# Optimization experiments

Measured on AMD Instinct MI355X. Metric: run time of the kernel, lower is better.

The kernel has to match this reference:

```python
import jax, jax.numpy as jnp
import numpy as np

B, H0, W0, C = 16, 56, 56, 96
NH, WS, SS = 3, 7, 3
HID, NCL, TAU = 384, 128, 0.5
EPS = 1e-6

def layernorm(x, g, b):
    m = jnp.mean(x, -1, keepdims=True)
    v = jnp.mean((x - m) ** 2, -1, keepdims=True)
    return (x - m) * jax.lax.rsqrt(v + 1e-5) * g + b

def setup_inputs() -> dict:
    key = jax.random.key(0)
    ks = jax.random.split(key, 16)
    s = lambda d: 1.0 / np.sqrt(d)
    return {
        "x": jax.random.normal(ks[0], (B, H0 * W0, C), jnp.float32),
        "norm1_g": jnp.ones((C,)), "norm1_b": jnp.zeros((C,)),
        "qkv_w": jax.random.normal(ks[1], (3 * C, C)) * s(C),
        "qkv_b": jnp.zeros((3 * C,)),
        "proj_w": jax.random.normal(ks[2], (C, C)) * s(C),
        "proj_b": jnp.zeros((C,)),
        "norm2_g": jnp.ones((C,)), "norm2_b": jnp.zeros((C,)),
        "ffn_norm_g": jnp.ones((C,)), "ffn_norm_b": jnp.zeros((C,)),
        "pin_w": jax.random.normal(ks[3], (HID, C)) * s(C),
        "pin_b": jnp.zeros((HID,)),
        "tm_inc": jax.random.normal(ks[4], (NCL, 2 * HID)) * 0.5,
        "tm_out": jax.random.normal(ks[5], (NCL, C)) * s(NCL),
        "gate": jnp.float32(0.5),
        "H": H0, "W": W0,
    }

def window_attention(win, qkv_w, qkv_b, proj_w, proj_b):
    N, T, Cc = win.shape
    hd = Cc // NH
    qkv = win @ qkv_w.T + qkv_b                      # [N, T, 3C]
    qkv = qkv.reshape(N, T, 3, NH, hd).transpose(2, 0, 3, 1, 4)
    q, k, v = qkv[0], qkv[1], qkv[2]                 # [N, nh, T, hd]
    attn = jax.nn.softmax(jnp.einsum('nhqd,nhkd->nhqk', q, k) * (hd ** -0.5), axis=-1)
    out = jnp.einsum('nhqk,nhkd->nhqd', attn, v).transpose(0, 2, 1, 3).reshape(N, T, Cc)
    return out @ proj_w.T + proj_b

def tm_ffn(x, ffn_norm_g, ffn_norm_b, pin_w, pin_b, tm_inc, tm_out, gate):
    # x: [B, T, C]
    Bb, T, Cc = x.shape
    y = jax.nn.sigmoid(layernorm(x, ffn_norm_g, ffn_norm_b) @ pin_w.T + pin_b)  # [B,T,HID]
    flat = y.reshape(Bb * T, HID)
    lits = jnp.clip(jnp.concatenate([flat, 1.0 - flat], axis=-1), EPS, 1.0)     # [N, 2*HID]
    m = jax.nn.sigmoid(tm_inc)
    hard = (m > TAU).astype(m.dtype)
    m_ste = m + jax.lax.stop_gradient(hard - m)      # binary via STE
    # binary mask -> conjunction prod_k l_k^{m_jk} = exp(log(l) @ m^T)
    clauses = jnp.exp(jnp.log(lits) @ m_ste.T)       # [N, NCL]
    logits = (clauses @ tm_out).reshape(Bb, T, Cc)
    g = jax.nn.sigmoid(gate)
    return g * logits + (1.0 - g) * jax.nn.sigmoid(logits)

def reference(x, norm1_g, norm1_b, qkv_w, qkv_b, proj_w, proj_b,
              norm2_g, norm2_b, ffn_norm_g, ffn_norm_b,
              pin_w, pin_b, tm_inc, tm_out, gate, H, W):
    Bb, L, Cc = x.shape
    shortcut = x
    y = layernorm(x, norm1_g, norm1_b).reshape(Bb, H, W, Cc)
    pad_h = (WS - H % WS) % WS
    pad_w = (WS - W % WS) % WS
    if pad_h or pad_w:
        y = jnp.pad(y, ((0, 0), (0, pad_h), (0, pad_w), (0, 0)))
    Hp, Wp = y.shape[1], y.shape[2]
    if SS > 0:
        y = jnp.roll(y, shift=(-SS, -SS), axis=(1, 2))
    # window partition
    y = y.reshape(Bb, Hp // WS, WS, Wp // WS, WS, Cc).transpose(0, 1, 3, 2, 4, 5)
    win = y.reshape(-1, WS * WS, Cc)
    a = window_attention(win, qkv_w, qkv_b, proj_w, proj_b)
    a = a.reshape(Bb, Hp // WS, Wp // WS, WS, WS, Cc)
    if SS > 0:
        a = jnp.roll(a, shift=(SS, SS), axis=(3, 4))
    # window reverse
    a = a.transpose(0, 1, 3, 2, 4, 5).reshape(Bb, Hp, Wp, Cc)
    if pad_h or pad_w:
        a = a[:, :H, :W, :]
    a = a.reshape(Bb, H * W, Cc)
    x1 = shortcut + a
    x2 = x1 + tm_ffn(layernorm(x1, norm2_g, norm2_b),
                     ffn_norm_g, ffn_norm_b, pin_w, pin_b, tm_inc, tm_out, gate)
    return x2
```

## Files before the change

### kernel.cpp

```cpp
#include <hip/hip_runtime.h>

#define NB 16
#define NHH 56
#define NWW 56
#define NC 96
#define NL (NHH*NWW)
#define NTOK (NB*NL)
#define WSZ 7
#define NT 49
#define SSH 3
#define NWIN 1024
#define HDIM 32
#define HID_ 384
#define NCL_ 128
#define NLIT 768
#define EPS_ 1e-6f
#define LOG_EPS -13.815510558f

typedef unsigned short u16;
typedef unsigned int   u32;
typedef __attribute__((ext_vector_type(8))) short short8;
typedef __attribute__((ext_vector_type(4))) float f32x4;

__device__ __forceinline__ float us2f(u16 u) {
  union { u32 u; float f; } x; x.u = ((u32)u) << 16; return x.f;
}
__device__ __forceinline__ u16 f2us(float f) {
  union { float f; u32 u; } x; x.f = f;
  u32 lsb = (x.u >> 16) & 1u;
  return (u16)((x.u + 0x7fffu + lsb) >> 16);
}
__device__ __forceinline__ float sigmoidf_(float x) { return 1.f / (1.f + __expf(-x)); }

__global__ __launch_bounds__(256) void k0_prep(const float* __restrict__ tm_inc,
                                               const float* __restrict__ pin_w,
                                               const float* __restrict__ tm_out,
                                               const float* __restrict__ qkv_w,
                                               const float* __restrict__ proj_w,
                                               u16* __restrict__ maskb,
                                               u16* __restrict__ pinwb,
                                               u16* __restrict__ tmoT,
                                               u16* __restrict__ qkvwb,
                                               u16* __restrict__ projwb) {
  int idx = blockIdx.x * 256 + threadIdx.x;
  if (idx < NCL_ * NLIT) {
    int c = idx / NLIT, q = idx - c * NLIT;
    int j = (q & 1) ? (q >> 1) + HID_ : (q >> 1);
    maskb[idx] = (tm_inc[(size_t)c * NLIT + j] > 0.f) ? (u16)0x3F80 : (u16)0;
  }
  if (idx < HID_ * NC)
    pinwb[idx] = f2us(pin_w[idx]);
  if (idx < NC * NCL_) {
    int c = idx / NCL_, k = idx - c * NCL_;
    tmoT[idx] = f2us(tm_out[(size_t)k * NC + c]);
  }
  if (idx < 3 * NC * NC)
    qkvwb[idx] = f2us(qkv_w[idx]);
  if (idx < NC * NC)
    projwb[idx] = f2us(proj_w[idx]);
}

__global__ __launch_bounds__(256, 4) void k2_attn(const float* __restrict__ x,
                                               const float* __restrict__ n1g,
                                               const float* __restrict__ n1b,
                                               const u16* __restrict__ qkvwb,
                                               const float* __restrict__ qkv_b,
                                               const u16* __restrict__ projwb,
                                               const float* __restrict__ proj_b,
                                               float* __restrict__ x1) {
  __shared__ __align__(16) u16 syb[64 * 104];
  __shared__ __align__(16) u16 sk [64 * 104];
  __shared__ __align__(16) u16 svT[96 * 72];
  const int tid  = threadIdx.x;
  const int wave = tid >> 6;
  const int lane = tid & 63;
  const int l16  = lane & 15;
  const int quad = lane >> 4;
  const int win  = blockIdx.x;
  const int t0   = wave * 16;
  const int bb = win >> 6, wl = win & 63;
  const int hbase = (wl >> 3) * WSZ, wbase = (wl & 7) * WSZ;

  {
    const int t = tid >> 2, s = tid & 3;
    if (t < NT) {
      int hp = hbase + t / WSZ, wp = wbase + t % WSZ;
      int h = hp + SSH; if (h >= NHH) h -= NHH;
      int w = wp + SSH; if (w >= NWW) w -= NWW;
      const float* xp = x + ((size_t)bb * NL + (size_t)h * NWW + w) * NC;
      float4 v[6];
      float sum = 0.f;
      #pragma unroll
      for (int k = 0; k < 6; ++k) {
        v[k] = *reinterpret_cast<const float4*>(xp + s * 4 + k * 16);
        sum += v[k].x + v[k].y + v[k].z + v[k].w;
      }
      sum += __shfl_xor(sum, 1); sum += __shfl_xor(sum, 2);
      float mean = sum * (1.f / 96.f);
      float ssq = 0.f;
      #pragma unroll
      for (int k = 0; k < 6; ++k) {
        float d0 = v[k].x - mean, d1 = v[k].y - mean;
        float d2 = v[k].z - mean, d3 = v[k].w - mean;
        ssq += d0 * d0 + d1 * d1 + d2 * d2 + d3 * d3;
      }
      ssq += __shfl_xor(ssq, 1); ssq += __shfl_xor(ssq, 2);
      float rstd = rsqrtf(ssq * (1.f / 96.f) + 1e-5f);
      #pragma unroll
      for (int k = 0; k < 6; ++k) {
        int c = s * 4 + k * 16;
        const float4 g4 = *reinterpret_cast<const float4*>(n1g + c);
        const float4 b4 = *reinterpret_cast<const float4*>(n1b + c);
        syb[t * 104 + c + 0] = f2us((v[k].x - mean) * rstd * g4.x + b4.x);
        syb[t * 104 + c + 1] = f2us((v[k].y - mean) * rstd * g4.y + b4.y);
        syb[t * 104 + c + 2] = f2us((v[k].z - mean) * rstd * g4.z + b4.z);
        syb[t * 104 + c + 3] = f2us((v[k].w - mean) * rstd * g4.w + b4.w);
      }
    } else {
      #pragma unroll
      for (int k = 0; k < 6; ++k) {
        int c = s * 4 + k * 16;
        syb[t * 104 + c + 0] = 0; syb[t * 104 + c + 1] = 0;
        syb[t * 104 + c + 2] = 0; syb[t * 104 + c + 3] = 0;
      }
    }
  }

  {
    short8 afr[3];
    #pragma unroll
    for (int ks = 0; ks < 3; ++ks)
      afr[ks] = *reinterpret_cast<const short8*>(&syb[(t0 + l16) * 104 + quad * 8 + ks * 32]);
    short8 rb[4][3];
    #pragma unroll
    for (int p = 0; p < 4; ++p)
      #pragma unroll
      for (int ks = 0; ks < 3; ++ks)
        rb[p][ks] = *reinterpret_cast<const short8*>(
            qkvwb + (size_t)(p * 16 + l16) * NC + quad * 8 + ks * 32);
    #pragma unroll
    for (int nt = 0; nt < 18; ++nt) {
      const int n0 = nt * 16;
      const float bias = qkv_b[n0 + l16];
      short8 b0 = rb[nt & 3][0], b1 = rb[nt & 3][1], b2 = rb[nt & 3][2];
      if (nt + 4 < 18) {
        #pragma unroll
        for (int ks = 0; ks < 3; ++ks)
          rb[nt & 3][ks] = *reinterpret_cast<const short8*>(
              qkvwb + (size_t)((nt + 4) * 16 + l16) * NC + quad * 8 + ks * 32);
      }
      f32x4 acc = {0.f, 0.f, 0.f, 0.f};
      acc = __builtin_amdgcn_mfma_f32_16x16x32_bf16(afr[0], b0, acc, 0, 0, 0);
      acc = __builtin_amdgcn_mfma_f32_16x16x32_bf16(afr[1], b1, acc, 0, 0, 0);
      acc = __builtin_amdgcn_mfma_f32_16x16x32_bf16(afr[2], b2, acc, 0, 0, 0);
      const int part = nt / 6;
      const int oc = n0 - part * 96 + l16;
      if (part < 2) {
        u16* dst = (part == 0) ? syb : sk;
        #pragma unroll
        for (int r = 0; r < 4; ++r)
          dst[(t0 + quad * 4 + r) * 104 + oc] = f2us(acc[r] + bias);
      } else {
        #pragma unroll
        for (int r = 0; r < 4; ++r)
          svT[oc * 72 + (t0 + quad * 4 + r)] = f2us(acc[r] + bias);
      }
    }
  }
  __syncthreads();

  u16* spw = sk + wave * 16 * 72;
  const float sscale = 0.17677669529663687f;
  short8 qf[3];
  f32x4 s[3][4];
  #pragma unroll
  for (int h = 0; h < 3; ++h)
    qf[h] = *reinterpret_cast<const short8*>(&syb[(t0 + l16) * 104 + h * HDIM + quad * 8]);
  #pragma unroll
  for (int h = 0; h < 3; ++h) {
    const int d0 = h * HDIM;
    #pragma unroll
    for (int nt = 0; nt < 4; ++nt) {
      short8 kf = *reinterpret_cast<const short8*>(&sk[(nt * 16 + l16) * 104 + d0 + quad * 8]);
      f32x4 a = {0.f, 0.f, 0.f, 0.f};
      s[h][nt] = __builtin_amdgcn_mfma_f32_16x16x32_bf16(qf[h], kf, a, 0, 0, 0);
    }
  }
  __syncthreads();
  #pragma unroll
  for (int h = 0; h < 3; ++h) {
    const int d0 = h * HDIM;
    #pragma unroll
    for (int nt = 0; nt < 4; ++nt)
      #pragma unroll
      for (int r = 0; r < 4; ++r) s[h][nt][r] *= sscale;
    if (l16 >= 1) {
      #pragma unroll
      for (int r = 0; r < 4; ++r) s[h][3][r] = -1e30f;
    }
    #pragma unroll
    for (int r = 0; r < 4; ++r) {
      float m = fmaxf(fmaxf(s[h][0][r], s[h][1][r]), fmaxf(s[h][2][r], s[h][3][r]));
      #pragma unroll
      for (int off = 8; off > 0; off >>= 1) m = fmaxf(m, __shfl_xor(m, off, 16));
      float e0 = __expf(s[h][0][r] - m), e1 = __expf(s[h][1][r] - m);
      float e2 = __expf(s[h][2][r] - m), e3 = __expf(s[h][3][r] - m);
      float sum = e0 + e1 + e2 + e3;
      #pragma unroll
      for (int off = 8; off > 0; off >>= 1) sum += __shfl_xor(sum, off, 16);
      float inv = 1.f / sum;
      const int row = quad * 4 + r;
      spw[row * 72 +      l16] = f2us(e0 * inv);
      spw[row * 72 + 16 + l16] = f2us(e1 * inv);
      spw[row * 72 + 32 + l16] = f2us(e2 * inv);
      spw[row * 72 + 48 + l16] = f2us(e3 * inv);
    }
    short8 pa[2];
    pa[0] = *reinterpret_cast<const short8*>(&spw[l16 * 72 + quad * 8]);
    pa[1] = *reinterpret_cast<const short8*>(&spw[l16 * 72 + 32 + quad * 8]);
    #pragma unroll
    for (int nt = 0; nt < 2; ++nt) {
      const int c0 = d0 + nt * 16;
      f32x4 acc = {0.f, 0.f, 0.f, 0.f};
      #pragma unroll
      for (int ks = 0; ks < 2; ++ks) {
        short8 vb = *reinterpret_cast<const short8*>(&svT[(c0 + l16) * 72 + ks * 32 + quad * 8]);
        acc = __builtin_amdgcn_mfma_f32_16x16x32_bf16(pa[ks], vb, acc, 0, 0, 0);
      }
      #pragma unroll
      for (int r = 0; r < 4; ++r)
        syb[(t0 + quad * 4 + r) * 104 + c0 + l16] = f2us(acc[r]);
    }
  }

  {
    short8 aa[3];
    #pragma unroll
    for (int ks = 0; ks < 3; ++ks)
      aa[ks] = *reinterpret_cast<const short8*>(&syb[(t0 + l16) * 104 + quad * 8 + ks * 32]);

    size_t tokr[4]; bool tval[4];
    #pragma unroll
    for (int r = 0; r < 4; ++r) {
      const int t = t0 + quad * 4 + r;
      tval[r] = (t < NT);
      int rr = t / WSZ + SSH; if (rr >= WSZ) rr -= WSZ;
      int qq = t % WSZ + SSH; if (qq >= WSZ) qq -= WSZ;
      tokr[r] = (size_t)bb * NL + (size_t)(hbase + rr) * NWW + (wbase + qq);
    }
    float xv[6][4];
    #pragma unroll
    for (int nt = 0; nt < 6; ++nt)
      #pragma unroll
      for (int r = 0; r < 4; ++r)
        xv[nt][r] = tval[r] ? x[tokr[r] * NC + nt * 16 + l16] : 0.f;

    short8 pbr[2][3];
    #pragma unroll
    for (int ks = 0; ks < 3; ++ks)
      pbr[0][ks] = *reinterpret_cast<const short8*>(
          projwb + (size_t)l16 * NC + quad * 8 + ks * 32);
    #pragma unroll
    for (int nt = 0; nt < 6; ++nt) {
      const int n0 = nt * 16;
      const float pb = proj_b[n0 + l16];
      short8 b0 = pbr[nt & 1][0], b1 = pbr[nt & 1][1], b2 = pbr[nt & 1][2];
      if (nt + 1 < 6) {
        #pragma unroll
        for (int ks = 0; ks < 3; ++ks)
          pbr[(nt + 1) & 1][ks] = *reinterpret_cast<const short8*>(
              projwb + (size_t)((nt + 1) * 16 + l16) * NC + quad * 8 + ks * 32);
      }
      f32x4 acc = {0.f, 0.f, 0.f, 0.f};
      acc = __builtin_amdgcn_mfma_f32_16x16x32_bf16(aa[0], b0, acc, 0, 0, 0);
      acc = __builtin_amdgcn_mfma_f32_16x16x32_bf16(aa[1], b1, acc, 0, 0, 0);
      acc = __builtin_amdgcn_mfma_f32_16x16x32_bf16(aa[2], b2, acc, 0, 0, 0);
      #pragma unroll
      for (int r = 0; r < 4; ++r) {
        if (tval[r])
          x1[tokr[r] * NC + n0 + l16] = xv[nt][r] + acc[r] + pb;
      }
    }
  }
}

__global__ __launch_bounds__(512, 6) void k4_ffn(const float* __restrict__ x1,
                                              const float* __restrict__ g2,
                                              const float* __restrict__ b2,
                                              const float* __restrict__ gf,
                                              const float* __restrict__ bf,
                                              const u16* __restrict__ pinwb,
                                              const float* __restrict__ pin_b,
                                              const u16* __restrict__ maskb,
                                              const u16* __restrict__ tmoT,
                                              const float* __restrict__ gate,
                                              float* __restrict__ out) {
  __shared__ __align__(16) u16 lit[32 * 776];
  u16* szb  = lit;
  u16* claT = lit;
  const int tid  = threadIdx.x;
  const int wave = tid >> 6;
  const int lane = tid & 63;
  const int l16  = lane & 15;
  const int quad = lane >> 4;
  const size_t tok0 = (size_t)blockIdx.x * 32;

  {
    const int t = tid >> 4, s = tid & 15;
    const float* xp = x1 + (tok0 + t) * NC;
    float2 v[3];
    float sum = 0.f;
    #pragma unroll
    for (int k = 0; k < 3; ++k) {
      const int c = s * 2 + k * 32;
      v[k] = *reinterpret_cast<const float2*>(xp + c);
      sum += v[k].x + v[k].y;
    }
    #pragma unroll
    for (int off = 8; off > 0; off >>= 1) sum += __shfl_xor(sum, off, 16);
    const float mean = sum * (1.f / 96.f);
    float ssq = 0.f;
    #pragma unroll
    for (int k = 0; k < 3; ++k) {
      float d0 = v[k].x - mean, d1 = v[k].y - mean;
      ssq += d0 * d0 + d1 * d1;
    }
    #pragma unroll
    for (int off = 8; off > 0; off >>= 1) ssq += __shfl_xor(ssq, off, 16);
    const float rstd = rsqrtf(ssq * (1.f / 96.f) + 1e-5f);
    float tv[6];
    float sum2 = 0.f;
    #pragma unroll
    for (int k = 0; k < 3; ++k) {
      const int c = s * 2 + k * 32;
      const float2 gg = *reinterpret_cast<const float2*>(g2 + c);
      const float2 bb = *reinterpret_cast<const float2*>(b2 + c);
      tv[2 * k]     = (v[k].x - mean) * rstd * gg.x + bb.x;
      tv[2 * k + 1] = (v[k].y - mean) * rstd * gg.y + bb.y;
      sum2 += tv[2 * k] + tv[2 * k + 1];
    }
    #pragma unroll
    for (int off = 8; off > 0; off >>= 1) sum2 += __shfl_xor(sum2, off, 16);
    const float mean2 = sum2 * (1.f / 96.f);
    float ssq2 = 0.f;
    #pragma unroll
    for (int k = 0; k < 3; ++k) {
      float d0 = tv[2 * k] - mean2, d1 = tv[2 * k + 1] - mean2;
      ssq2 += d0 * d0 + d1 * d1;
    }
    #pragma unroll
    for (int off = 8; off > 0; off >>= 1) ssq2 += __shfl_xor(ssq2, off, 16);
    const float rstd2 = rsqrtf(ssq2 * (1.f / 96.f) + 1e-5f);
    #pragma unroll
    for (int k = 0; k < 3; ++k) {
      const int c = s * 2 + k * 32;
      const float2 gg = *reinterpret_cast<const float2*>(gf + c);
      const float2 bb = *reinterpret_cast<const float2*>(bf + c);
      u16 lo = f2us((tv[2 * k]     - mean2) * rstd2 * gg.x + bb.x);
      u16 hi = f2us((tv[2 * k + 1] - mean2) * rstd2 * gg.y + bb.y);
      *reinterpret_cast<u32*>(&szb[t * 104 + c]) = (u32)lo | ((u32)hi << 16);
    }
  }
  __syncthreads();

  const float gv = sigmoidf_(gate[0]);

  short8 a_pin[2][3];
  #pragma unroll
  for (int mt = 0; mt < 2; ++mt)
    #pragma unroll
    for (int ks = 0; ks < 3; ++ks)
      a_pin[mt][ks] = *reinterpret_cast<const short8*>(
          &szb[(mt * 16 + l16) * 104 + quad * 8 + ks * 32]);
  __syncthreads();

  {
    float pbias[3];
    #pragma unroll
    for (int i = 0; i < 3; ++i) pbias[i] = pin_b[(wave * 3 + i) * 16 + l16];
    short8 pb[3][3];
    #pragma unroll
    for (int i = 0; i < 3; ++i)
      #pragma unroll
      for (int ks = 0; ks < 3; ++ks)
        pb[i][ks] = *reinterpret_cast<const short8*>(
            pinwb + (size_t)((wave * 3 + i) * 16 + l16) * NC + quad * 8 + ks * 32);
    #pragma unroll
    for (int i = 0; i < 3; ++i) {
      f32x4 acc0 = {0.f, 0.f, 0.f, 0.f}, acc1 = {0.f, 0.f, 0.f, 0.f};
      acc0 = __builtin_amdgcn_mfma_f32_16x16x32_bf16(a_pin[0][0], pb[i][0], acc0, 0, 0, 0);
      acc1 = __builtin_amdgcn_mfma_f32_16x16x32_bf16(a_pin[1][0], pb[i][0], acc1, 0, 0, 0);
      acc0 = __builtin_amdgcn_mfma_f32_16x16x32_bf16(a_pin[0][1], pb[i][1], acc0, 0, 0, 0);
      acc1 = __builtin_amdgcn_mfma_f32_16x16x32_bf16(a_pin[1][1], pb[i][1], acc1, 0, 0, 0);
      acc0 = __builtin_amdgcn_mfma_f32_16x16x32_bf16(a_pin[0][2], pb[i][2], acc0, 0, 0, 0);
      acc1 = __builtin_amdgcn_mfma_f32_16x16x32_bf16(a_pin[1][2], pb[i][2], acc1, 0, 0, 0);
      const int o = (wave * 3 + i) * 16 + l16;
      const float pbv = pbias[i];
      #pragma unroll
      for (int r = 0; r < 4; ++r) {
        const float a0 = acc0[r] + pbv;
        const float sp0 = fmaxf(a0, 0.f) + __logf(1.f + __expf(-fabsf(a0)));
        const float a1 = acc1[r] + pbv;
        const float sp1 = fmaxf(a1, 0.f) + __logf(1.f + __expf(-fabsf(a1)));
        const int ta = quad * 4 + r, tb = 16 + quad * 4 + r;
        const u16 lo0 = f2us(fmaxf(a0 - sp0, LOG_EPS));
        const u16 hi0 = f2us(fmaxf(-sp0, LOG_EPS));
        const u16 lo1 = f2us(fmaxf(a1 - sp1, LOG_EPS));
        const u16 hi1 = f2us(fmaxf(-sp1, LOG_EPS));
        *reinterpret_cast<u32*>(&lit[ta * 776 + 2 * o]) = (u32)lo0 | ((u32)hi0 << 16);
        *reinterpret_cast<u32*>(&lit[tb * 776 + 2 * o]) = (u32)lo1 | ((u32)hi1 << 16);
      }
    }
  }
  __syncthreads();

  float xr[2][4];
  if (wave < 6) {
    const int c = wave * 16 + l16;
    #pragma unroll
    for (int r = 0; r < 4; ++r) {
      xr[0][r] = x1[(tok0 + quad * 4 + r) * NC + c];
      xr[1][r] = x1[(tok0 + 16 + quad * 4 + r) * NC + c];
    }
  }

  {
    const int ct = wave;
    const u16* bp0 = maskb + (size_t)(ct * 16 + l16) * NLIT + quad * 8;
    short8 rb0[8];
    #pragma unroll
    for (int p = 0; p < 8; ++p)
      rb0[p] = *reinterpret_cast<const short8*>(bp0 + p * 32);
    f32x4 c00 = {0.f, 0.f, 0.f, 0.f}, c10 = {0.f, 0.f, 0.f, 0.f};
    #pragma unroll
    for (int ks = 0; ks < 24; ++ks) {
      const int k0 = ks * 32 + quad * 8;
      short8 a0 = *reinterpret_cast<const short8*>(&lit[l16 * 776 + k0]);
      short8 a1 = *reinterpret_cast<const short8*>(&lit[(16 + l16) * 776 + k0]);
      short8 b0 = rb0[ks & 7];
      if (ks + 8 < 24)
        rb0[ks & 7] = *reinterpret_cast<const short8*>(bp0 + (ks + 8) * 32);
      c00 = __builtin_amdgcn_mfma_f32_16x16x32_bf16(a0, b0, c00, 0, 0, 0);
      c10 = __builtin_amdgcn_mfma_f32_16x16x32_bf16(a1, b0, c10, 0, 0, 0);
    }
    float e0[4], e1[4];
    #pragma unroll
    for (int r = 0; r < 4; ++r) { e0[r] = __expf(c00[r]); e1[r] = __expf(c10[r]); }
    __syncthreads();
    #pragma unroll
    for (int r = 0; r < 4; ++r) {
      const int ta = quad * 4 + r, tb = 16 + quad * 4 + r;
      claT[ta * 136 + ct * 16 + l16] = f2us(e0[r]);
      claT[tb * 136 + ct * 16 + l16] = f2us(e1[r]);
    }
  }
  __syncthreads();

  if (wave < 6) {
    const int nt = wave;
    short8 btm[4];
    #pragma unroll
    for (int ks = 0; ks < 4; ++ks)
      btm[ks] = *reinterpret_cast<const short8*>(
          tmoT + (size_t)(nt * 16 + l16) * NCL_ + ks * 32 + quad * 8);
    f32x4 acc0 = {0.f, 0.f, 0.f, 0.f}, acc1 = {0.f, 0.f, 0.f, 0.f};
    #pragma unroll
    for (int ks = 0; ks < 4; ++ks) {
      const int k0 = ks * 32 + quad * 8;
      short8 a0 = *reinterpret_cast<const short8*>(&claT[l16 * 136 + k0]);
      short8 a1 = *reinterpret_cast<const short8*>(&claT[(16 + l16) * 136 + k0]);
      acc0 = __builtin_amdgcn_mfma_f32_16x16x32_bf16(a0, btm[ks], acc0, 0, 0, 0);
      acc1 = __builtin_amdgcn_mfma_f32_16x16x32_bf16(a1, btm[ks], acc1, 0, 0, 0);
    }
    const int c = nt * 16 + l16;
    #pragma unroll
    for (int r = 0; r < 4; ++r) {
      const int ta = quad * 4 + r, tb = 16 + quad * 4 + r;
      float lg0 = acc0[r], lg1 = acc1[r];
      out[(tok0 + ta) * NC + c] = xr[0][r] + gv * lg0 + (1.f - gv) * sigmoidf_(lg0);
      out[(tok0 + tb) * NC + c] = xr[1][r] + gv * lg1 + (1.f - gv) * sigmoidf_(lg1);
    }
  }
}

extern "C" void kernel_launch(void* const* d_in, const int* in_sizes, int n_in,
                              void* d_out, int out_size, void* d_ws, size_t ws_size,
                              hipStream_t stream) {
  (void)in_sizes; (void)n_in; (void)out_size; (void)ws_size;
  const float* x      = (const float*)d_in[0];
  const float* n1g    = (const float*)d_in[1];
  const float* n1b    = (const float*)d_in[2];
  const float* qkv_w  = (const float*)d_in[3];
  const float* qkv_b  = (const float*)d_in[4];
  const float* proj_w = (const float*)d_in[5];
  const float* proj_b = (const float*)d_in[6];
  const float* n2g    = (const float*)d_in[7];
  const float* n2b    = (const float*)d_in[8];
  const float* fng    = (const float*)d_in[9];
  const float* fnb    = (const float*)d_in[10];
  const float* pin_w  = (const float*)d_in[11];
  const float* pin_b  = (const float*)d_in[12];
  const float* tm_inc = (const float*)d_in[13];
  const float* tm_out = (const float*)d_in[14];
  const float* gate   = (const float*)d_in[15];

  float* x1 = (float*)d_ws;
  u16* maskb = (u16*)(x1 + (size_t)NTOK * NC);
  u16* pinwb = maskb + NCL_ * NLIT;
  u16* tmoT  = pinwb + HID_ * NC;
  u16* qkvwb = tmoT + NC * NCL_;
  u16* projwb= qkvwb + 3 * NC * NC;

  hipLaunchKernelGGL(k0_prep, dim3(384), dim3(256), 0, stream,
                     tm_inc, pin_w, tm_out, qkv_w, proj_w, maskb, pinwb, tmoT, qkvwb, projwb);
  hipLaunchKernelGGL(k2_attn, dim3(NWIN), dim3(256), 0, stream,
                     x, n1g, n1b, qkvwb, qkv_b, projwb, proj_b, x1);
  hipLaunchKernelGGL(k4_ffn, dim3(NTOK / 32), dim3(512), 0, stream,
                     x1, n2g, n2b, fng, fnb, pinwb, pin_b, maskb, tmoT, gate, (float*)d_out);
}
```

Measured before the change: 188.1 us.

## Halve FFN block tile to 16 tokens with 4 waves and rebalanced work

The FFN kernel now handles 16 tokens per block with 256 threads instead of 32 tokens with 512, which halves the shared-memory tile and doubles the grid. Each wave computes 6 pin-projection tiles, 2 clause tiles and 1-2 output tiles, with register double-buffering of weight loads. The aim is higher occupancy and less LDS per block. The cost is that each block reloads the mask and pin weights for only 16 tokens, so reuse of those weights per block is halved and global/L2 traffic rises.

New measurement: 226.2 us. 20.2% more time.

```diff
diff --git a/kernel.cpp b/kernel.cpp
--- a/kernel.cpp
+++ b/kernel.cpp
@@ -284,7 +284,7 @@
   }
 }
 
-__global__ __launch_bounds__(512, 6) void k4_ffn(const float* __restrict__ x1,
+__global__ __launch_bounds__(256, 6) void k4_ffn(const float* __restrict__ x1,
                                               const float* __restrict__ g2,
                                               const float* __restrict__ b2,
                                               const float* __restrict__ gf,
@@ -295,7 +295,7 @@
                                               const u16* __restrict__ tmoT,
                                               const float* __restrict__ gate,
                                               float* __restrict__ out) {
-  __shared__ __align__(16) u16 lit[32 * 776];
+  __shared__ __align__(16) u16 lit[16 * 776];
   u16* szb  = lit;
   u16* claT = lit;
   const int tid  = threadIdx.x;
@@ -303,7 +303,7 @@
   const int lane = tid & 63;
   const int l16  = lane & 15;
   const int quad = lane >> 4;
-  const size_t tok0 = (size_t)blockIdx.x * 32;
+  const size_t tok0 = (size_t)blockIdx.x * 16;
 
   {
     const int t = tid >> 4, s = tid & 15;
@@ -365,120 +365,121 @@
 
   const float gv = sigmoidf_(gate[0]);
 
-  short8 a_pin[2][3];
+  short8 a_pin[3];
   #pragma unroll
-  for (int mt = 0; mt < 2; ++mt)
-    #pragma unroll
-    for (int ks = 0; ks < 3; ++ks)
-      a_pin[mt][ks] = *reinterpret_cast<const short8*>(
-          &szb[(mt * 16 + l16) * 104 + quad * 8 + ks * 32]);
+  for (int ks = 0; ks < 3; ++ks)
+    a_pin[ks] = *reinterpret_cast<const short8*>(
+        &szb[l16 * 104 + quad * 8 + ks * 32]);
   __syncthreads();
 
   {
-    float pbias[3];
-    #pragma unroll
-    for (int i = 0; i < 3; ++i) pbias[i] = pin_b[(wave * 3 + i) * 16 + l16];
-    short8 pb[3][3];
-    #pragma unroll
-    for (int i = 0; i < 3; ++i)
+    short8 pb[2][3];
+    #pragma unroll
+    for (int p = 0; p < 2; ++p)
       #pragma unroll
       for (int ks = 0; ks < 3; ++ks)
-        pb[i][ks] = *reinterpret_cast<const short8*>(
-            pinwb + (size_t)((wave * 3 + i) * 16 + l16) * NC + quad * 8 + ks * 32);
-    #pragma unroll
-    for (int i = 0; i < 3; ++i) {
-      f32x4 acc0 = {0.f, 0.f, 0.f, 0.f}, acc1 = {0.f, 0.f, 0.f, 0.f};
-      acc0 = __builtin_amdgcn_mfma_f32_16x16x32_bf16(a_pin[0][0], pb[i][0], acc0, 0, 0, 0);
-      acc1 = __builtin_amdgcn_mfma_f32_16x16x32_bf16(a_pin[1][0], pb[i][0], acc1, 0, 0, 0);
-      acc0 = __builtin_amdgcn_mfma_f32_16x16x32_bf16(a_pin[0][1], pb[i][1], acc0, 0, 0, 0);
-      acc1 = __builtin_amdgcn_mfma_f32_16x16x32_bf16(a_pin[1][1], pb[i][1], acc1, 0, 0, 0);
-      acc0 = __builtin_amdgcn_mfma_f32_16x16x32_bf16(a_pin[0][2], pb[i][2], acc0, 0, 0, 0);
-      acc1 = __builtin_amdgcn_mfma_f32_16x16x32_bf16(a_pin[1][2], pb[i][2], acc1, 0, 0, 0);
-      const int o = (wave * 3 + i) * 16 + l16;
-      const float pbv = pbias[i];
+        pb[p][ks] = *reinterpret_cast<const short8*>(
+            pinwb + (size_t)((wave * 6 + p) * 16 + l16) * NC + quad * 8 + ks * 32);
+    #pragma unroll
+    for (int i = 0; i < 6; ++i) {
+      const int o = (wave * 6 + i) * 16 + l16;
+      const float pbv = pin_b[o];
+      short8 b0 = pb[i & 1][0], b1 = pb[i & 1][1], b2 = pb[i & 1][2];
+      if (i + 2 < 6) {
+        #pragma unroll
+        for (int ks = 0; ks < 3; ++ks)
+          pb[i & 1][ks] = *reinterpret_cast<const short8*>(
+              pinwb + (size_t)((wave * 6 + i + 2) * 16 + l16) * NC + quad * 8 + ks * 32);
+      }
+      f32x4 acc = {0.f, 0.f, 0.f, 0.f};
+      acc = __builtin_amdgcn_mfma_f32_16x16x32_bf16(a_pin[0], b0, acc, 0, 0, 0);
+      acc = __builtin_amdgcn_mfma_f32_16x16x32_bf16(a_pin[1], b1, acc, 0, 0, 0);
+      acc = __builtin_amdgcn_mfma_f32_16x16x32_bf16(a_pin[2], b2, acc, 0, 0, 0);
       #pragma unroll
       for (int r = 0; r < 4; ++r) {
-        const float a0 = acc0[r] + pbv;
+        const float a0 = acc[r] + pbv;
         const float sp0 = fmaxf(a0, 0.f) + __logf(1.f + __expf(-fabsf(a0)));
-        const float a1 = acc1[r] + pbv;
-        const float sp1 = fmaxf(a1, 0.f) + __logf(1.f + __expf(-fabsf(a1)));
-        const int ta = quad * 4 + r, tb = 16 + quad * 4 + r;
+        const int ta = quad * 4 + r;
         const u16 lo0 = f2us(fmaxf(a0 - sp0, LOG_EPS));
         const u16 hi0 = f2us(fmaxf(-sp0, LOG_EPS));
-        const u16 lo1 = f2us(fmaxf(a1 - sp1, LOG_EPS));
-        const u16 hi1 = f2us(fmaxf(-sp1, LOG_EPS));
         *reinterpret_cast<u32*>(&lit[ta * 776 + 2 * o]) = (u32)lo0 | ((u32)hi0 << 16);
-        *reinterpret_cast<u32*>(&lit[tb * 776 + 2 * o]) = (u32)lo1 | ((u32)hi1 << 16);
       }
     }
   }
   __syncthreads();
 
+  const int nnt = (wave < 2) ? 2 : 1;
+  int ntl[2]; ntl[0] = wave; ntl[1] = wave + 4;
   float xr[2][4];
-  if (wave < 6) {
-    const int c = wave * 16 + l16;
-    #pragma unroll
-    for (int r = 0; r < 4; ++r) {
-      xr[0][r] = x1[(tok0 + quad * 4 + r) * NC + c];
-      xr[1][r] = x1[(tok0 + 16 + quad * 4 + r) * NC + c];
+  #pragma unroll
+  for (int j = 0; j < 2; ++j) {
+    if (j < nnt) {
+      const int c = ntl[j] * 16 + l16;
+      #pragma unroll
+      for (int r = 0; r < 4; ++r)
+        xr[j][r] = x1[(tok0 + quad * 4 + r) * NC + c];
     }
   }
 
   {
-    const int ct = wave;
-    const u16* bp0 = maskb + (size_t)(ct * 16 + l16) * NLIT + quad * 8;
-    short8 rb0[8];
-    #pragma unroll
-    for (int p = 0; p < 8; ++p)
+    const int ct0 = 2 * wave;
+    const u16* bp0 = maskb + (size_t)(ct0 * 16 + l16) * NLIT + quad * 8;
+    const u16* bp1 = maskb + (size_t)((ct0 + 1) * 16 + l16) * NLIT + quad * 8;
+    short8 rb0[4], rb1[4];
+    #pragma unroll
+    for (int p = 0; p < 4; ++p) {
       rb0[p] = *reinterpret_cast<const short8*>(bp0 + p * 32);
-    f32x4 c00 = {0.f, 0.f, 0.f, 0.f}, c10 = {0.f, 0.f, 0.f, 0.f};
+      rb1[p] = *reinterpret_cast<const short8*>(bp1 + p * 32);
+    }
+    f32x4 c0 = {0.f, 0.f, 0.f, 0.f}, c1 = {0.f, 0.f, 0.f, 0.f};
     #pragma unroll
     for (int ks = 0; ks < 24; ++ks) {
       const int k0 = ks * 32 + quad * 8;
       short8 a0 = *reinterpret_cast<const short8*>(&lit[l16 * 776 + k0]);
-      short8 a1 = *reinterpret_cast<const short8*>(&lit[(16 + l16) * 776 + k0]);
-      short8 b0 = rb0[ks & 7];
-      if (ks + 8 < 24)
-        rb0[ks & 7] = *reinterpret_cast<const short8*>(bp0 + (ks + 8) * 32);
-      c00 = __builtin_amdgcn_mfma_f32_16x16x32_bf16(a0, b0, c00, 0, 0, 0);
-      c10 = __builtin_amdgcn_mfma_f32_16x16x32_bf16(a1, b0, c10, 0, 0, 0);
+      short8 b0 = rb0[ks & 3], b1 = rb1[ks & 3];
+      if (ks + 4 < 24) {
+        rb0[ks & 3] = *reinterpret_cast<const short8*>(bp0 + (ks + 4) * 32);
+        rb1[ks & 3] = *reinterpret_cast<const short8*>(bp1 + (ks + 4) * 32);
+      }
+      c0 = __builtin_amdgcn_mfma_f32_16x16x32_bf16(a0, b0, c0, 0, 0, 0);
+      c1 = __builtin_amdgcn_mfma_f32_16x16x32_bf16(a0, b1, c1, 0, 0, 0);
     }
     float e0[4], e1[4];
     #pragma unroll
-    for (int r = 0; r < 4; ++r) { e0[r] = __expf(c00[r]); e1[r] = __expf(c10[r]); }
+    for (int r = 0; r < 4; ++r) { e0[r] = __expf(c0[r]); e1[r] = __expf(c1[r]); }
     __syncthreads();
     #pragma unroll
     for (int r = 0; r < 4; ++r) {
-      const int ta = quad * 4 + r, tb = 16 + quad * 4 + r;
-      claT[ta * 136 + ct * 16 + l16] = f2us(e0[r]);
-      claT[tb * 136 + ct * 16 + l16] = f2us(e1[r]);
+      const int ta = quad * 4 + r;
+      claT[ta * 136 + ct0 * 16 + l16]        = f2us(e0[r]);
+      claT[ta * 136 + (ct0 + 1) * 16 + l16]  = f2us(e1[r]);
     }
   }
   __syncthreads();
 
-  if (wave < 6) {
-    const int nt = wave;
-    short8 btm[4];
-    #pragma unroll
-    for (int ks = 0; ks < 4; ++ks)
-      btm[ks] = *reinterpret_cast<const short8*>(
-          tmoT + (size_t)(nt * 16 + l16) * NCL_ + ks * 32 + quad * 8);
-    f32x4 acc0 = {0.f, 0.f, 0.f, 0.f}, acc1 = {0.f, 0.f, 0.f, 0.f};
-    #pragma unroll
-    for (int ks = 0; ks < 4; ++ks) {
-      const int k0 = ks * 32 + quad * 8;
-      short8 a0 = *reinterpret_cast<const short8*>(&claT[l16 * 136 + k0]);
-      short8 a1 = *reinterpret_cast<const short8*>(&claT[(16 + l16) * 136 + k0]);
-      acc0 = __builtin_amdgcn_mfma_f32_16x16x32_bf16(a0, btm[ks], acc0, 0, 0, 0);
-      acc1 = __builtin_amdgcn_mfma_f32_16x16x32_bf16(a1, btm[ks], acc1, 0, 0, 0);
-    }
-    const int c = nt * 16 + l16;
-    #pragma unroll
-    for (int r = 0; r < 4; ++r) {
-      const int ta = quad * 4 + r, tb = 16 + quad * 4 + r;
-      float lg0 = acc0[r], lg1 = acc1[r];
-      out[(tok0 + ta) * NC + c] = xr[0][r] + gv * lg0 + (1.f - gv) * sigmoidf_(lg0);
-      out[(tok0 + tb) * NC + c] = xr[1][r] + gv * lg1 + (1.f - gv) * sigmoidf_(lg1);
+  #pragma unroll
+  for (int j = 0; j < 2; ++j) {
+    if (j < nnt) {
+      const int nt = ntl[j];
+      short8 btm[4];
+      #pragma unroll
+      for (int ks = 0; ks < 4; ++ks)
+        btm[ks] = *reinterpret_cast<const short8*>(
+            tmoT + (size_t)(nt * 16 + l16) * NCL_ + ks * 32 + quad * 8);
+      f32x4 acc = {0.f, 0.f, 0.f, 0.f};
+      #pragma unroll
+      for (int ks = 0; ks < 4; ++ks) {
+        const int k0 = ks * 32 + quad * 8;
+        short8 a0 = *reinterpret_cast<const short8*>(&claT[l16 * 136 + k0]);
+        acc = __builtin_amdgcn_mfma_f32_16x16x32_bf16(a0, btm[ks], acc, 0, 0, 0);
+      }
+      const int c = nt * 16 + l16;
+      #pragma unroll
+      for (int r = 0; r < 4; ++r) {
+        const int ta = quad * 4 + r;
+        float lg = acc[r];
+        out[(tok0 + ta) * NC + c] = xr[j][r] + gv * lg + (1.f - gv) * sigmoidf_(lg);
+      }
     }
   }
 }
@@ -515,6 +516,6 @@
                      tm_inc, pin_w, tm_out, qkv_w, proj_w, maskb, pinwb, tmoT, qkvwb, projwb);
   hipLaunchKernelGGL(k2_attn, dim3(NWIN), dim3(256), 0, stream,
                      x, n1g, n1b, qkvwb, qkv_b, projwb, proj_b, x1);
-  hipLaunchKernelGGL(k4_ffn, dim3(NTOK / 32), dim3(512), 0, stream,
+  hipLaunchKernelGGL(k4_ffn, dim3(NTOK / 16), dim3(256), 0, stream,
                      x1, n2g, n2b, fng, fnb, pinwb, pin_b, maskb, tmoT, gate, (float*)d_out);
 }
```

## Split fused FFN kernel into pin-projection and clause kernels via global literals

Applied to the files above, without the earlier changes.

The fused FFN kernel is split in two. The first kernel computes the double layernorm, the pin projection and the log-literals, and writes them as bf16 to a workspace buffer. The second kernel reads those literals from global memory for the clause GEMM, then applies exp and the output projection. This is meant to cut LDS use and register pressure per kernel and raise occupancy. In exchange it adds about 38 MB of global write and read traffic plus an extra launch. The split path runs only when the workspace is large enough; otherwise the old fused kernel is used.

Result: slower. 273.5 us (+45.4%).

```diff
diff --git a/kernel.cpp b/kernel.cpp
--- a/kernel.cpp
+++ b/kernel.cpp
@@ -284,6 +284,218 @@
   }
 }
 
+__global__ __launch_bounds__(512, 4) void k4a_pin(const float* __restrict__ x1,
+                                              const float* __restrict__ g2,
+                                              const float* __restrict__ b2,
+                                              const float* __restrict__ gf,
+                                              const float* __restrict__ bf,
+                                              const u16* __restrict__ pinwb,
+                                              const float* __restrict__ pin_b,
+                                              u16* __restrict__ litg) {
+  __shared__ __align__(16) u16 szb[32 * 104];
+  const int tid  = threadIdx.x;
+  const int wave = tid >> 6;
+  const int lane = tid & 63;
+  const int l16  = lane & 15;
+  const int quad = lane >> 4;
+  const size_t tok0 = (size_t)blockIdx.x * 32;
+
+  {
+    const int t = tid >> 4, s = tid & 15;
+    const float* xp = x1 + (tok0 + t) * NC;
+    float2 v[3];
+    float sum = 0.f;
+    #pragma unroll
+    for (int k = 0; k < 3; ++k) {
+      const int c = s * 2 + k * 32;
+      v[k] = *reinterpret_cast<const float2*>(xp + c);
+      sum += v[k].x + v[k].y;
+    }
+    #pragma unroll
+    for (int off = 8; off > 0; off >>= 1) sum += __shfl_xor(sum, off, 16);
+    const float mean = sum * (1.f / 96.f);
+    float ssq = 0.f;
+    #pragma unroll
+    for (int k = 0; k < 3; ++k) {
+      float d0 = v[k].x - mean, d1 = v[k].y - mean;
+      ssq += d0 * d0 + d1 * d1;
+    }
+    #pragma unroll
+    for (int off = 8; off > 0; off >>= 1) ssq += __shfl_xor(ssq, off, 16);
+    const float rstd = rsqrtf(ssq * (1.f / 96.f) + 1e-5f);
+    float tv[6];
+    float sum2 = 0.f;
+    #pragma unroll
+    for (int k = 0; k < 3; ++k) {
+      const int c = s * 2 + k * 32;
+      const float2 gg = *reinterpret_cast<const float2*>(g2 + c);
+      const float2 bb = *reinterpret_cast<const float2*>(b2 + c);
+      tv[2 * k]     = (v[k].x - mean) * rstd * gg.x + bb.x;
+      tv[2 * k + 1] = (v[k].y - mean) * rstd * gg.y + bb.y;
+      sum2 += tv[2 * k] + tv[2 * k + 1];
+    }
+    #pragma unroll
+    for (int off = 8; off > 0; off >>= 1) sum2 += __shfl_xor(sum2, off, 16);
+    const float mean2 = sum2 * (1.f / 96.f);
+    float ssq2 = 0.f;
+    #pragma unroll
+    for (int k = 0; k < 3; ++k) {
+      float d0 = tv[2 * k] - mean2, d1 = tv[2 * k + 1] - mean2;
+      ssq2 += d0 * d0 + d1 * d1;
+    }
+    #pragma unroll
+    for (int off = 8; off > 0; off >>= 1) ssq2 += __shfl_xor(ssq2, off, 16);
+    const float rstd2 = rsqrtf(ssq2 * (1.f / 96.f) + 1e-5f);
+    #pragma unroll
+    for (int k = 0; k < 3; ++k) {
+      const int c = s * 2 + k * 32;
+      const float2 gg = *reinterpret_cast<const float2*>(gf + c);
+      const float2 bb = *reinterpret_cast<const float2*>(bf + c);
+      u16 lo = f2us((tv[2 * k]     - mean2) * rstd2 * gg.x + bb.x);
+      u16 hi = f2us((tv[2 * k + 1] - mean2) * rstd2 * gg.y + bb.y);
+      *reinterpret_cast<u32*>(&szb[t * 104 + c]) = (u32)lo | ((u32)hi << 16);
+    }
+  }
+  __syncthreads();
+
+  short8 a_pin[2][3];
+  #pragma unroll
+  for (int mt = 0; mt < 2; ++mt)
+    #pragma unroll
+    for (int ks = 0; ks < 3; ++ks)
+      a_pin[mt][ks] = *reinterpret_cast<const short8*>(
+          &szb[(mt * 16 + l16) * 104 + quad * 8 + ks * 32]);
+
+  {
+    float pbias[3];
+    #pragma unroll
+    for (int i = 0; i < 3; ++i) pbias[i] = pin_b[(wave * 3 + i) * 16 + l16];
+    short8 pb[3][3];
+    #pragma unroll
+    for (int i = 0; i < 3; ++i)
+      #pragma unroll
+      for (int ks = 0; ks < 3; ++ks)
+        pb[i][ks] = *reinterpret_cast<const short8*>(
+            pinwb + (size_t)((wave * 3 + i) * 16 + l16) * NC + quad * 8 + ks * 32);
+    #pragma unroll
+    for (int i = 0; i < 3; ++i) {
+      f32x4 acc0 = {0.f, 0.f, 0.f, 0.f}, acc1 = {0.f, 0.f, 0.f, 0.f};
+      acc0 = __builtin_amdgcn_mfma_f32_16x16x32_bf16(a_pin[0][0], pb[i][0], acc0, 0, 0, 0);
+      acc1 = __builtin_amdgcn_mfma_f32_16x16x32_bf16(a_pin[1][0], pb[i][0], acc1, 0, 0, 0);
+      acc0 = __builtin_amdgcn_mfma_f32_16x16x32_bf16(a_pin[0][1], pb[i][1], acc0, 0, 0, 0);
+      acc1 = __builtin_amdgcn_mfma_f32_16x16x32_bf16(a_pin[1][1], pb[i][1], acc1, 0, 0, 0);
+      acc0 = __builtin_amdgcn_mfma_f32_16x16x32_bf16(a_pin[0][2], pb[i][2], acc0, 0, 0, 0);
+      acc1 = __builtin_amdgcn_mfma_f32_16x16x32_bf16(a_pin[1][2], pb[i][2], acc1, 0, 0, 0);
+      const int o = (wave * 3 + i) * 16 + l16;
+      const float pbv = pbias[i];
+      #pragma unroll
+      for (int r = 0; r < 4; ++r) {
+        const float a0 = acc0[r] + pbv;
+        const float sp0 = fmaxf(a0, 0.f) + __logf(1.f + __expf(-fabsf(a0)));
+        const float a1 = acc1[r] + pbv;
+        const float sp1 = fmaxf(a1, 0.f) + __logf(1.f + __expf(-fabsf(a1)));
+        const int ta = quad * 4 + r, tb = 16 + quad * 4 + r;
+        const u16 lo0 = f2us(fmaxf(a0 - sp0, LOG_EPS));
+        const u16 hi0 = f2us(fmaxf(-sp0, LOG_EPS));
+        const u16 lo1 = f2us(fmaxf(a1 - sp1, LOG_EPS));
+        const u16 hi1 = f2us(fmaxf(-sp1, LOG_EPS));
+        *reinterpret_cast<u32*>(litg + (tok0 + ta) * NLIT + 2 * o) = (u32)lo0 | ((u32)hi0 << 16);
+        *reinterpret_cast<u32*>(litg + (tok0 + tb) * NLIT + 2 * o) = (u32)lo1 | ((u32)hi1 << 16);
+      }
+    }
+  }
+}
+
+__global__ __launch_bounds__(512, 4) void k4b_cla(const float* __restrict__ x1,
+                                              const u16* __restrict__ litg,
+                                              const u16* __restrict__ maskb,
+                                              const u16* __restrict__ tmoT,
+                                              const float* __restrict__ gate,
+                                              float* __restrict__ out) {
+  __shared__ __align__(16) u16 claT[32 * 136];
+  const int tid  = threadIdx.x;
+  const int wave = tid >> 6;
+  const int lane = tid & 63;
+  const int l16  = lane & 15;
+  const int quad = lane >> 4;
+  const size_t tok0 = (size_t)blockIdx.x * 32;
+
+  float xr[2][4];
+  if (wave < 6) {
+    const int c = wave * 16 + l16;
+    #pragma unroll
+    for (int r = 0; r < 4; ++r) {
+      xr[0][r] = x1[(tok0 + quad * 4 + r) * NC + c];
+      xr[1][r] = x1[(tok0 + 16 + quad * 4 + r) * NC + c];
+    }
+  }
+
+  {
+    const int ct = wave;
+    const u16* bp0 = maskb + (size_t)(ct * 16 + l16) * NLIT + quad * 8;
+    const u16* ap0 = litg + (tok0 + l16) * NLIT + quad * 8;
+    const u16* ap1 = litg + (tok0 + 16 + l16) * NLIT + quad * 8;
+    short8 rb0[8];
+    #pragma unroll
+    for (int p = 0; p < 8; ++p)
+      rb0[p] = *reinterpret_cast<const short8*>(bp0 + p * 32);
+    short8 ra0[2], ra1[2];
+    #pragma unroll
+    for (int p = 0; p < 2; ++p) {
+      ra0[p] = *reinterpret_cast<const short8*>(ap0 + p * 32);
+      ra1[p] = *reinterpret_cast<const short8*>(ap1 + p * 32);
+    }
+    f32x4 c00 = {0.f, 0.f, 0.f, 0.f}, c10 = {0.f, 0.f, 0.f, 0.f};
+    #pragma unroll
+    for (int ks = 0; ks < 24; ++ks) {
+      short8 a0 = ra0[ks & 1], a1 = ra1[ks & 1];
+      short8 b0 = rb0[ks & 7];
+      if (ks + 2 < 24) {
+        ra0[ks & 1] = *reinterpret_cast<const short8*>(ap0 + (ks + 2) * 32);
+        ra1[ks & 1] = *reinterpret_cast<const short8*>(ap1 + (ks + 2) * 32);
+      }
+      if (ks + 8 < 24)
+        rb0[ks & 7] = *reinterpret_cast<const short8*>(bp0 + (ks + 8) * 32);
+      c00 = __builtin_amdgcn_mfma_f32_16x16x32_bf16(a0, b0, c00, 0, 0, 0);
+      c10 = __builtin_amdgcn_mfma_f32_16x16x32_bf16(a1, b0, c10, 0, 0, 0);
+    }
+    #pragma unroll
+    for (int r = 0; r < 4; ++r) {
+      const int ta = quad * 4 + r, tb = 16 + quad * 4 + r;
+      claT[ta * 136 + ct * 16 + l16] = f2us(__expf(c00[r]));
+      claT[tb * 136 + ct * 16 + l16] = f2us(__expf(c10[r]));
+    }
+  }
+  __syncthreads();
+
+  if (wave < 6) {
+    const float gv = sigmoidf_(gate[0]);
+    const int nt = wave;
+    short8 btm[4];
+    #pragma unroll
+    for (int ks = 0; ks < 4; ++ks)
+      btm[ks] = *reinterpret_cast<const short8*>(
+          tmoT + (size_t)(nt * 16 + l16) * NCL_ + ks * 32 + quad * 8);
+    f32x4 acc0 = {0.f, 0.f, 0.f, 0.f}, acc1 = {0.f, 0.f, 0.f, 0.f};
+    #pragma unroll
+    for (int ks = 0; ks < 4; ++ks) {
+      const int k0 = ks * 32 + quad * 8;
+      short8 a0 = *reinterpret_cast<const short8*>(&claT[l16 * 136 + k0]);
+      short8 a1 = *reinterpret_cast<const short8*>(&claT[(16 + l16) * 136 + k0]);
+      acc0 = __builtin_amdgcn_mfma_f32_16x16x32_bf16(a0, btm[ks], acc0, 0, 0, 0);
+      acc1 = __builtin_amdgcn_mfma_f32_16x16x32_bf16(a1, btm[ks], acc1, 0, 0, 0);
+    }
+    const int c = nt * 16 + l16;
+    #pragma unroll
+    for (int r = 0; r < 4; ++r) {
+      const int ta = quad * 4 + r, tb = 16 + quad * 4 + r;
+      float lg0 = acc0[r], lg1 = acc1[r];
+      out[(tok0 + ta) * NC + c] = xr[0][r] + gv * lg0 + (1.f - gv) * sigmoidf_(lg0);
+      out[(tok0 + tb) * NC + c] = xr[1][r] + gv * lg1 + (1.f - gv) * sigmoidf_(lg1);
+    }
+  }
+}
+
 __global__ __launch_bounds__(512, 6) void k4_ffn(const float* __restrict__ x1,
                                               const float* __restrict__ g2,
                                               const float* __restrict__ b2,
@@ -486,7 +698,7 @@
 extern "C" void kernel_launch(void* const* d_in, const int* in_sizes, int n_in,
                               void* d_out, int out_size, void* d_ws, size_t ws_size,
                               hipStream_t stream) {
-  (void)in_sizes; (void)n_in; (void)out_size; (void)ws_size;
+  (void)in_sizes; (void)n_in; (void)out_size;
   const float* x      = (const float*)d_in[0];
   const float* n1g    = (const float*)d_in[1];
   const float* n1b    = (const float*)d_in[2];
@@ -510,11 +722,24 @@
   u16* tmoT  = pinwb + HID_ * NC;
   u16* qkvwb = tmoT + NC * NCL_;
   u16* projwb= qkvwb + 3 * NC * NC;
+  u16* litg  = projwb + NC * NC;
+
+  const size_t need_split =
+      (size_t)NTOK * NC * 4 +
+      (size_t)(NCL_ * NLIT + HID_ * NC + NC * NCL_ + 3 * NC * NC + NC * NC) * 2 +
+      (size_t)NTOK * NLIT * 2;
 
   hipLaunchKernelGGL(k0_prep, dim3(384), dim3(256), 0, stream,
                      tm_inc, pin_w, tm_out, qkv_w, proj_w, maskb, pinwb, tmoT, qkvwb, projwb);
   hipLaunchKernelGGL(k2_attn, dim3(NWIN), dim3(256), 0, stream,
                      x, n1g, n1b, qkvwb, qkv_b, projwb, proj_b, x1);
-  hipLaunchKernelGGL(k4_ffn, dim3(NTOK / 32), dim3(512), 0, stream,
-                     x1, n2g, n2b, fng, fnb, pinwb, pin_b, maskb, tmoT, gate, (float*)d_out);
+  if (ws_size >= need_split) {
+    hipLaunchKernelGGL(k4a_pin, dim3(NTOK / 32), dim3(512), 0, stream,
+                       x1, n2g, n2b, fng, fnb, pinwb, pin_b, litg);
+    hipLaunchKernelGGL(k4b_cla, dim3(NTOK / 32), dim3(512), 0, stream,
+                       x1, litg, maskb, tmoT, gate, (float*)d_out);
+  } else {
+    hipLaunchKernelGGL(k4_ffn, dim3(NTOK / 32), dim3(512), 0, stream,
+                       x1, n2g, n2b, fng, fnb, pinwb, pin_b, maskb, tmoT, gate, (float*)d_out);
+  }
 }
```
